# Performance work log

Hardware: AMD Instinct MI355X
Metric: run time of the kernel (lower is better)

The kernel has to match this reference:

```python
import jax, jax.numpy as jnp
import numpy as np

D_MODEL = 512
D_STATE = 128
D_CONV = 4
D_INNER = 1024
HEADDIM = 64
NHEADS = 16
CONV_DIM = D_INNER + 2 * D_STATE          # 1280
D_IN_PROJ = 2 * D_INNER + 2 * D_STATE + NHEADS  # 2320
N_LAYER = 28
VOCAB = 256
EPS = 1e-5
BATCH = 16
SEQ = 768


def _rms(x, w):
    return x * jax.lax.rsqrt(jnp.mean(x * x, axis=-1, keepdims=True) + EPS) * w


def _ssd(x, dt, A, Bm, Cm):
    # x [B,L,H,P], dt [B,L,H], A [H], Bm/Cm [B,L,N] (ngroups=1, broadcast over heads)
    Bb, L, H, P = x.shape
    N = Bm.shape[-1]
    dA = jnp.exp(dt * A)          # [B,L,H] discrete decay
    dBx = dt[..., None] * x       # [B,L,H,P]

    def step(h, t):
        dA_t, dBx_t, B_t, C_t = t
        # h: [B,H,P,N]
        h = dA_t[:, :, None, None] * h + dBx_t[..., None] * B_t[:, None, None, :]
        y = jnp.einsum('bhpn,bn->bhp', h, C_t)
        return h, y

    h0 = jnp.zeros((Bb, H, P, N), x.dtype)
    xs = (jnp.moveaxis(dA, 1, 0), jnp.moveaxis(dBx, 1, 0),
          jnp.moveaxis(Bm, 1, 0), jnp.moveaxis(Cm, 1, 0))
    _, ys = jax.lax.scan(step, h0, xs)
    return jnp.moveaxis(ys, 0, 1)  # [B,L,H,P]


def _mamba2(u, p):
    # u: [B,L,D_MODEL]
    Bb, L, _ = u.shape
    zxbcdt = u @ p['in_proj_w'].T                      # [B,L,2320]
    z = zxbcdt[..., :D_INNER]
    xBC = zxbcdt[..., D_INNER:D_INNER + CONV_DIM]
    dt = jax.nn.softplus(zxbcdt[..., D_INNER + CONV_DIM:] + p['dt_bias'])  # [B,L,H]
    # causal depthwise conv1d (kernel 4) + silu
    xp = jnp.pad(xBC, ((0, 0), (D_CONV - 1, 0), (0, 0)))
    conv = sum(xp[:, k:k + L, :] * p['conv_w'][:, k] for k in range(D_CONV)) + p['conv_b']
    xBC = jax.nn.silu(conv)
    x = xBC[..., :D_INNER].reshape(Bb, L, NHEADS, HEADDIM)
    Bm = xBC[..., D_INNER:D_INNER + D_STATE]
    Cm = xBC[..., D_INNER + D_STATE:]
    A = -jnp.exp(p['A_log'])                           # [H]
    y = _ssd(x, dt, A, Bm, Cm) + p['D'][None, None, :, None] * x
    y = y.reshape(Bb, L, D_INNER)
    # RMSNormGated (norm_before_gate=False): norm(y * silu(z)) * w
    y = _rms(y * jax.nn.silu(z), p['gnorm_w'])
    return y @ p['out_proj_w'].T


def _forward(tokens, targets, params):
    hidden = params['embedding'][tokens]               # [B,L,D]
    residual = jnp.zeros_like(hidden)

    layer_params = {k: params[k] for k in
                    ('in_proj_w', 'conv_w', 'conv_b', 'dt_bias', 'A_log',
                     'D', 'gnorm_w', 'out_proj_w', 'block_norm_w')}

    def layer(carry, lp):
        h, res = carry
        res = h + res
        h = _rms(res, lp['block_norm_w'])
        h = _mamba2(h, lp)
        return (h, res), None

    (hidden, residual), _ = jax.lax.scan(layer, (hidden, residual), layer_params)
    hidden = _rms(hidden + residual, params['norm_f_w'])
    logits = hidden @ params['embedding'].T            # tied lm_head
    logp = jax.nn.log_softmax(logits, axis=-1)
    loss = -jnp.mean(jnp.take_along_axis(logp, targets[..., None], axis=-1))
    return logits, loss


def setup_inputs():
    key = jax.random.key(0)
    ks = jax.random.split(key, 12)
    tokens = jax.random.randint(ks[0], (BATCH, SEQ), 0, VOCAB, dtype=jnp.int32)
    targets = jax.random.randint(ks[1], (BATCH, SEQ), 0, VOCAB, dtype=jnp.int32)
    embedding = jax.random.normal(ks[2], (VOCAB, D_MODEL), jnp.float32) * 0.02
    in_proj_w = jax.random.normal(ks[3], (N_LAYER, D_IN_PROJ, D_MODEL), jnp.float32) * (D_MODEL ** -0.5)
    conv_w = jax.random.normal(ks[4], (N_LAYER, CONV_DIM, D_CONV), jnp.float32) * 0.2
    conv_b = jnp.zeros((N_LAYER, CONV_DIM), jnp.float32)
    dt0 = jnp.exp(jax.random.uniform(ks[5], (N_LAYER, NHEADS)) * (np.log(0.1) - np.log(1e-3)) + np.log(1e-3))
    dt_bias = dt0 + jnp.log(-jnp.expm1(-dt0))          # inverse softplus
    A_log = jnp.log(jax.random.uniform(ks[6], (N_LAYER, NHEADS), minval=1.0, maxval=16.0))
    Dp = jnp.ones((N_LAYER, NHEADS), jnp.float32)
    gnorm_w = jnp.ones((N_LAYER, D_INNER), jnp.float32)
    out_proj_w = jax.random.normal(ks[7], (N_LAYER, D_MODEL, D_INNER), jnp.float32) * (D_INNER ** -0.5 / np.sqrt(N_LAYER))
    block_norm_w = jnp.ones((N_LAYER, D_MODEL), jnp.float32)
    norm_f_w = jnp.ones((D_MODEL,), jnp.float32)
    return {'tokens': tokens, 'targets': targets, 'embedding': embedding,
            'in_proj_w': in_proj_w, 'conv_w': conv_w, 'conv_b': conv_b,
            'dt_bias': dt_bias, 'A_log': A_log, 'D': Dp, 'gnorm_w': gnorm_w,
            'out_proj_w': out_proj_w, 'block_norm_w': block_norm_w, 'norm_f_w': norm_f_w}


def reference(tokens, targets, embedding, in_proj_w, conv_w, conv_b, dt_bias,
              A_log, D, gnorm_w, out_proj_w, block_norm_w, norm_f_w):
    params = {'embedding': embedding, 'in_proj_w': in_proj_w, 'conv_w': conv_w,
              'conv_b': conv_b, 'dt_bias': dt_bias, 'A_log': A_log, 'D': D,
              'gnorm_w': gnorm_w, 'out_proj_w': out_proj_w,
              'block_norm_w': block_norm_w, 'norm_f_w': norm_f_w}
    return _forward(tokens, targets, params)
```

## Files before the change

### kernel.cpp

```cpp
#include <hip/hip_runtime.h>
#include <hip/hip_bf16.h>
#include <math.h>

#define BATCH   16
#define SEQ     768
#define DMODEL  512
#define DSTATE  128
#define DINNER  1024
#define NHEADS  16
#define HEADDIM 64
#define CONVDIM 1280
#define DINPROJ 2320
#define DINPROJP 2432
#define DTBASE  2304
#define NLAYER  28
#define VOCABSZ 256
#define NROWS   (BATCH*SEQ)
#define EPSV    1e-5f
#define NCH     8
#define CH      96
#define STATESZ (HEADDIM*DSTATE)

typedef __hip_bfloat16 bf16_t;
typedef __attribute__((ext_vector_type(8))) __bf16 bf16x8;
typedef __attribute__((ext_vector_type(4))) float floatx4;

__device__ __forceinline__ float siluf(float v) { return v / (1.f + expf(-v)); }

__device__ __forceinline__ void gload_lds16(const bf16_t* g, bf16_t* l) {
  __builtin_amdgcn_global_load_lds(
      (const __attribute__((address_space(1))) unsigned int*)g,
      (__attribute__((address_space(3))) unsigned int*)l, 16, 0, 0);
}

__global__ __launch_bounds__(256) void embed_kernel(const int* __restrict__ tok,
    const float* __restrict__ emb, float* __restrict__ hid, float* __restrict__ res,
    bf16_t* __restrict__ w_emb_bf) {
  int i = blockIdx.x * 256 + threadIdx.x;
  const int total = NROWS * DMODEL;
  if (i < total) {
    int r = i >> 9;
    int d = i & (DMODEL - 1);
    hid[i] = emb[(size_t)tok[r] * DMODEL + d];
    res[i] = 0.f;
  } else {
    int j = i - total;
    if (j < VOCABSZ * DMODEL) w_emb_bf[j] = __float2bfloat16(emb[j]);
  }
}

__global__ __launch_bounds__(256) void cvt_weights_kernel(const float* __restrict__ ipw,
    const float* __restrict__ opw, bf16_t* __restrict__ win, bf16_t* __restrict__ wout) {
  int i = blockIdx.x * 256 + threadIdx.x;
  const int n1 = DINPROJP * DMODEL;
  if (i < n1) {
    int row = i >> 9, col = i & (DMODEL - 1);
    float v = (row < DINPROJ) ? ipw[(size_t)row * DMODEL + col] : 0.f;
    win[i] = __float2bfloat16(v);
  } else {
    int j = i - n1;
    if (j < DMODEL * DINNER) wout[j] = __float2bfloat16(opw[j]);
  }
}

__global__ __launch_bounds__(128) void prenorm_kernel(const float* __restrict__ h,
    float* __restrict__ res, const float* __restrict__ w, bf16_t* __restrict__ xn) {
  int row = blockIdx.x;
  int tid = threadIdx.x;
  const float4* h4 = (const float4*)(h + (size_t)row * DMODEL);
  float4* r4 = (float4*)(res + (size_t)row * DMODEL);
  float4 v = r4[tid];
  float4 a = h4[tid];
  v.x += a.x; v.y += a.y; v.z += a.z; v.w += a.w;
  r4[tid] = v;
  float ss = v.x * v.x + v.y * v.y + v.z * v.z + v.w * v.w;
  #pragma unroll
  for (int o = 32; o > 0; o >>= 1) ss += __shfl_down(ss, o);
  __shared__ float wred[2];
  if ((tid & 63) == 0) wred[tid >> 6] = ss;
  __syncthreads();
  float tot = wred[0] + wred[1];
  float scale = rsqrtf(tot / (float)DMODEL + EPSV);
  const float4* w4 = (const float4*)w;
  float4 wv = w4[tid];
  union { bf16_t b[4]; uint2 u; } pk;
  pk.b[0] = __float2bfloat16(v.x * scale * wv.x);
  pk.b[1] = __float2bfloat16(v.y * scale * wv.y);
  pk.b[2] = __float2bfloat16(v.z * scale * wv.z);
  pk.b[3] = __float2bfloat16(v.w * scale * wv.w);
  ((uint2*)(xn + (size_t)row * DMODEL))[tid] = pk.u;
}

template<int BN, typename TO>
__global__ __launch_bounds__(256) void gemm_bf16_bt(const bf16_t* __restrict__ A,
    const bf16_t* __restrict__ B, TO* __restrict__ C, float* __restrict__ aux,
    int M, int N, int K) {
  constexpr int JF = BN / 32;
  __shared__ bf16_t As[128 * 32];
  __shared__ bf16_t Bs[BN * 32];
  int tid = threadIdx.x;
  int m0 = blockIdx.y * 128;
  int n0 = blockIdx.x * BN;
  int w = tid >> 6, lane = tid & 63;
  int wm = (w >> 1) * 64, wn = (w & 1) * (BN / 2);
  int l16 = lane & 15, lq = lane >> 4;
  floatx4 acc[4][JF];
  #pragma unroll
  for (int i = 0; i < 4; ++i)
    #pragma unroll
    for (int j = 0; j < JF; ++j)
      acc[i][j] = (floatx4){0.f, 0.f, 0.f, 0.f};
  int arow0 = tid >> 2, ak0 = (tid & 3) * 8;
  const bf16_t* Abase = A + (size_t)m0 * K;
  const bf16_t* Bbase = B + (size_t)n0 * K;
  bf16_t* AsW = As + (w << 9);
  bf16_t* BsW = Bs + (w << 9);
  for (int k0 = 0; k0 < K; k0 += 32) {
    __syncthreads();
    gload_lds16(Abase + (size_t)arow0 * K + k0 + ak0, AsW);
    gload_lds16(Abase + (size_t)(arow0 + 64) * K + k0 + ak0, AsW + 2048);
    gload_lds16(Bbase + (size_t)arow0 * K + k0 + ak0, BsW);
    if (BN == 128)
      gload_lds16(Bbase + (size_t)(arow0 + 64) * K + k0 + ak0, BsW + 2048);
    __syncthreads();
    bf16x8 af[4], bfr[JF];
    #pragma unroll
    for (int i = 0; i < 4; ++i)
      af[i] = *(const bf16x8*)(As + (wm + i * 16 + l16) * 32 + lq * 8);
    #pragma unroll
    for (int j = 0; j < JF; ++j)
      bfr[j] = *(const bf16x8*)(Bs + (wn + j * 16 + l16) * 32 + lq * 8);
    #pragma unroll
    for (int i = 0; i < 4; ++i)
      #pragma unroll
      for (int j = 0; j < JF; ++j)
        acc[i][j] = __builtin_amdgcn_mfma_f32_16x16x32_bf16(af[i], bfr[j], acc[i][j], 0, 0, 0);
  }
  #pragma unroll
  for (int i = 0; i < 4; ++i) {
    #pragma unroll
    for (int j = 0; j < JF; ++j) {
      int n = n0 + wn + j * 16 + l16;
      if (n < N) {
        int mb = m0 + wm + i * 16 + lq * 4;
        #pragma unroll
        for (int r = 0; r < 4; ++r) {
          float vv = acc[i][j][r];
          if constexpr (sizeof(TO) == 2)
            C[(size_t)(mb + r) * N + n] = __float2bfloat16(vv);
          else
            C[(size_t)(mb + r) * N + n] = vv;
          if (aux && n >= DTBASE)
            aux[(size_t)(mb + r) * NHEADS + (n - DTBASE)] = vv;
        }
      }
    }
  }
}

__global__ __launch_bounds__(320) void convdt_kernel(const bf16_t* __restrict__ zx,
    const float* __restrict__ dtcol, const float* __restrict__ cw,
    const float* __restrict__ cb, const float* __restrict__ dt_bias,
    const float* __restrict__ A_log, bf16_t* __restrict__ out,
    float* __restrict__ dt, float* __restrict__ ldA) {
  int bl0 = blockIdx.x * 4;
  int t0 = bl0 % SEQ;
  int tid = threadIdx.x;
  int c = tid * 4;
  const bf16_t* base = zx + (size_t)bl0 * DINPROJ + DINNER + c;
  float4 v[7];
  #pragma unroll
  for (int k = 0; k < 7; ++k) {
    int tt = t0 + k - 3;
    if (tt >= 0) {
      union { ushort4 u; bf16_t b[4]; } q;
      q.u = *(const ushort4*)(base + (ptrdiff_t)(k - 3) * DINPROJ);
      v[k] = make_float4(__bfloat162float(q.b[0]), __bfloat162float(q.b[1]),
                         __bfloat162float(q.b[2]), __bfloat162float(q.b[3]));
    } else {
      v[k] = make_float4(0.f, 0.f, 0.f, 0.f);
    }
  }
  float4 w0 = *(const float4*)(cw + (size_t)(c + 0) * 4);
  float4 w1 = *(const float4*)(cw + (size_t)(c + 1) * 4);
  float4 w2 = *(const float4*)(cw + (size_t)(c + 2) * 4);
  float4 w3 = *(const float4*)(cw + (size_t)(c + 3) * 4);
  float4 bias = *(const float4*)(cb + c);
  const float* w0f = (const float*)&w0;
  const float* w1f = (const float*)&w1;
  const float* w2f = (const float*)&w2;
  const float* w3f = (const float*)&w3;
  #pragma unroll
  for (int j = 0; j < 4; ++j) {
    float4 acc = bias;
    #pragma unroll
    for (int k = 0; k < 4; ++k) {
      float4 vv = v[j + k];
      acc.x += vv.x * w0f[k];
      acc.y += vv.y * w1f[k];
      acc.z += vv.z * w2f[k];
      acc.w += vv.w * w3f[k];
    }
    union { ushort4 u; bf16_t b[4]; } pk;
    pk.b[0] = __float2bfloat16(siluf(acc.x));
    pk.b[1] = __float2bfloat16(siluf(acc.y));
    pk.b[2] = __float2bfloat16(siluf(acc.z));
    pk.b[3] = __float2bfloat16(siluf(acc.w));
    *(ushort4*)(out + (size_t)(bl0 + j) * CONVDIM + c) = pk.u;
  }
  if (tid < 64) {
    int j = tid >> 4, h = tid & 15;
    int bl = bl0 + j;
    float vv = dtcol[(size_t)bl * NHEADS + h] + dt_bias[h];
    float sp = fmaxf(vv, 0.f) + log1pf(expf(-fabsf(vv)));
    float Ah = -expf(A_log[h]);
    dt[bl * NHEADS + h] = sp;
    ldA[bl * NHEADS + h] = sp * Ah;
  }
}

__global__ __launch_bounds__(512) void scan_mfma_kernel(const bf16_t* __restrict__ conv,
    const float* __restrict__ dtb, const float* __restrict__ ldAb,
    const float* __restrict__ Dp, float* __restrict__ y,
    float* __restrict__ state, float* __restrict__ chunkprod,
    float* __restrict__ cumb) {
  const int c  = blockIdx.x;
  const int b  = blockIdx.y >> 1;
  const int h0 = (blockIdx.y & 1) * 8;
  const int tid  = threadIdx.x;
  const int w    = tid >> 6;
  const int lane = tid & 63;
  const size_t row0 = (size_t)(b * SEQ + c * CH);

  __shared__ __align__(16) bf16_t Bb[96 * 136];
  __shared__ __align__(16) bf16_t Cb[96 * 136];
  __shared__ __align__(16) bf16_t Pl[96 * 104];
  __shared__ __align__(16) bf16_t xT[64 * 104];
  __shared__ __align__(16) bf16_t BTw[128 * 104];
  __shared__ float ldas[8][96];
  __shared__ float dts[8][96];
  __shared__ float cums[8][96];
  __shared__ float wts[8][96];

  for (int i = tid; i < 96 * 32; i += 512) {
    int t = i >> 5, g = i & 31;
    bf16x8 v = *(const bf16x8*)(conv + (row0 + t) * CONVDIM + DINNER + g * 8);
    if (g < 16) *(bf16x8*)(Bb + t * 136 + g * 8) = v;
    else        *(bf16x8*)(Cb + t * 136 + (g - 16) * 8) = v;
  }
  for (int i = tid; i < 768; i += 512) {
    int hh = i & 7, t = i >> 3;
    size_t gi = (row0 + t) * NHEADS + h0 + hh;
    dts[hh][t]  = dtb[gi];
    ldas[hh][t] = ldAb[gi];
  }
  __syncthreads();
  if (tid < 8) {
    float cacc = 0.f;
    for (int t = 0; t < 96; ++t) { cacc += ldas[tid][t]; cums[tid][t] = cacc; }
  }
  __syncthreads();
  for (int i = tid; i < 768; i += 512) {
    int hh = i & 7, t = i >> 3;
    wts[hh][t] = expf(cums[hh][95] - cums[hh][t]) * dts[hh][t];
    cumb[(row0 + t) * NHEADS + h0 + hh] = cums[hh][t];
  }
  if (tid < 8)
    chunkprod[(b * NHEADS + h0 + tid) * NCH + c] = expf(cums[tid][95]);

  floatx4 gacc[5];
  #pragma unroll
  for (int it = 0; it < 5; ++it) gacc[it] = (floatx4){0.f, 0.f, 0.f, 0.f};
  const int l16 = lane & 15, lk = (lane >> 4) << 3;
  #pragma unroll
  for (int it = 0; it < 5; ++it) {
    int tt = w + it * 8;
    int ti = (tt < 36) ? (tt / 6) : 0;
    int si = (tt < 36) ? (tt % 6) : 0;
    #pragma unroll
    for (int ks = 0; ks < 4; ++ks) {
      bf16x8 a = *(const bf16x8*)(Cb + (ti * 16 + l16) * 136 + ks * 32 + lk);
      bf16x8 bb = *(const bf16x8*)(Bb + (si * 16 + l16) * 136 + ks * 32 + lk);
      gacc[it] = __builtin_amdgcn_mfma_f32_16x16x32_bf16(a, bb, gacc[it], 0, 0, 0);
    }
  }

  for (int hh = 0; hh < 8; ++hh) {
    __syncthreads();
    for (int i = tid; i < 768; i += 512) {
      int t = i >> 3, p8 = (i & 7) * 8;
      union { bf16x8 v8; unsigned short s[8]; } u;
      u.v8 = *(const bf16x8*)(conv + (row0 + t) * CONVDIM + (h0 + hh) * HEADDIM + p8);
      #pragma unroll
      for (int r = 0; r < 8; ++r)
        ((unsigned short*)xT)[(p8 + r) * 104 + t] = u.s[r];
    }
    for (int i = tid; i < 128 * 96; i += 512) {
      int n = i / 96, t = i - n * 96;
      float bv = __bfloat162float(Bb[t * 136 + n]);
      BTw[n * 104 + t] = __float2bfloat16(wts[hh][t] * bv);
    }
    #pragma unroll
    for (int it = 0; it < 5; ++it) {
      int tt = w + it * 8;
      if (tt < 36) {
        int ti = tt / 6, si = tt % 6;
        int scol = si * 16 + l16;
        #pragma unroll
        for (int r = 0; r < 4; ++r) {
          int trow = ti * 16 + ((lane >> 4) << 2) + r;
          float pv = 0.f;
          if (scol <= trow)
            pv = expf(cums[hh][trow] - cums[hh][scol]) * dts[hh][scol] * gacc[it][r];
          Pl[trow * 104 + scol] = __float2bfloat16(pv);
        }
      }
    }
    __syncthreads();
    float Dh = Dp[h0 + hh];
    #pragma unroll
    for (int it = 0; it < 3; ++it) {
      int tt = w + it * 8;
      int ti = tt >> 2, pi = tt & 3;
      floatx4 acc = (floatx4){0.f, 0.f, 0.f, 0.f};
      #pragma unroll
      for (int ks = 0; ks < 3; ++ks) {
        bf16x8 a = *(const bf16x8*)(Pl + (ti * 16 + l16) * 104 + ks * 32 + lk);
        bf16x8 bb = *(const bf16x8*)(xT + (pi * 16 + l16) * 104 + ks * 32 + lk);
        acc = __builtin_amdgcn_mfma_f32_16x16x32_bf16(a, bb, acc, 0, 0, 0);
      }
      int p = pi * 16 + l16;
      #pragma unroll
      for (int r = 0; r < 4; ++r) {
        int t = ti * 16 + ((lane >> 4) << 2) + r;
        float xg = __bfloat162float(conv[(row0 + t) * CONVDIM + (h0 + hh) * HEADDIM + p]);
        y[((row0 + t) * NHEADS + h0 + hh) * HEADDIM + p] = acc[r] + Dh * xg;
      }
    }
    size_t sb = ((size_t)(b * NHEADS + h0 + hh) * NCH + c) * STATESZ;
    #pragma unroll
    for (int it = 0; it < 4; ++it) {
      int tt = w + it * 8;
      int ni = tt >> 2, pi = tt & 3;
      floatx4 acc = (floatx4){0.f, 0.f, 0.f, 0.f};
      #pragma unroll
      for (int ks = 0; ks < 3; ++ks) {
        bf16x8 a = *(const bf16x8*)(BTw + (ni * 16 + l16) * 104 + ks * 32 + lk);
        bf16x8 bb = *(const bf16x8*)(xT + (pi * 16 + l16) * 104 + ks * 32 + lk);
        acc = __builtin_amdgcn_mfma_f32_16x16x32_bf16(a, bb, acc, 0, 0, 0);
      }
      int p = pi * 16 + l16;
      #pragma unroll
      for (int r = 0; r < 4; ++r) {
        int n = ni * 16 + ((lane >> 4) << 2) + r;
        state[sb + (size_t)n * HEADDIM + p] = acc[r];
      }
    }
  }
}

__global__ __launch_bounds__(256) void state_combine_kernel(float* __restrict__ state,
    const float* __restrict__ cprod) {
  int bh = blockIdx.y;
  int sl = blockIdx.x;
  int tid = threadIdx.x;
  float4* slab = (float4*)(state + (size_t)bh * NCH * STATESZ) + sl * 256 + tid;
  const float* pc = cprod + bh * NCH;
  float4 H = make_float4(0.f, 0.f, 0.f, 0.f);
  for (int c = 1; c < NCH; ++c) {
    float P = pc[c - 1];
    float4* sp = slab + (size_t)(c - 1) * (STATESZ / 4);
    float4 S = *sp;
    H.x = P * H.x + S.x; H.y = P * H.y + S.y;
    H.z = P * H.z + S.z; H.w = P * H.w + S.w;
    *sp = H;
  }
}

__global__ __launch_bounds__(512) void ycorr_mfma_kernel(const bf16_t* __restrict__ conv,
    const float* __restrict__ cumb, const float* __restrict__ state,
    float* __restrict__ y) {
  const int c  = blockIdx.x + 1;
  const int b  = blockIdx.y >> 1;
  const int h0 = (blockIdx.y & 1) * 8;
  const int tid  = threadIdx.x;
  const int w    = tid >> 6;
  const int lane = tid & 63;
  const int l16 = lane & 15, lk = (lane >> 4) << 3;
  const size_t row0 = (size_t)(b * SEQ + c * CH);

  __shared__ __align__(16) bf16_t Cb[96 * 136];
  __shared__ __align__(16) bf16_t HT[64 * 136];
  __shared__ float cAs[8][96];

  for (int i = tid; i < 96 * 16; i += 512) {
    int t = i >> 4, g = i & 15;
    bf16x8 v = *(const bf16x8*)(conv + (row0 + t) * CONVDIM + DINNER + DSTATE + g * 8);
    *(bf16x8*)(Cb + t * 136 + g * 8) = v;
  }
  for (int i = tid; i < 768; i += 512) {
    int hh = i & 7, t = i >> 3;
    cAs[hh][t] = expf(cumb[(row0 + t) * NHEADS + h0 + hh]);
  }

  for (int hh = 0; hh < 8; ++hh) {
    __syncthreads();
    const float* Hs = state + ((size_t)(b * NHEADS + h0 + hh) * NCH + (c - 1)) * STATESZ;
    for (int i = tid; i < STATESZ; i += 512) {
      int n = i >> 6, p = i & 63;
      HT[p * 136 + n] = __float2bfloat16(Hs[i]);
    }
    __syncthreads();
    #pragma unroll
    for (int it = 0; it < 3; ++it) {
      int tt = w + it * 8;
      int ti = tt >> 2, pi = tt & 3;
      floatx4 acc = (floatx4){0.f, 0.f, 0.f, 0.f};
      #pragma unroll
      for (int ks = 0; ks < 4; ++ks) {
        bf16x8 a = *(const bf16x8*)(Cb + (ti * 16 + l16) * 136 + ks * 32 + lk);
        bf16x8 bb = *(const bf16x8*)(HT + (pi * 16 + l16) * 136 + ks * 32 + lk);
        acc = __builtin_amdgcn_mfma_f32_16x16x32_bf16(a, bb, acc, 0, 0, 0);
      }
      int p = pi * 16 + l16;
      #pragma unroll
      for (int r = 0; r < 4; ++r) {
        int t = ti * 16 + ((lane >> 4) << 2) + r;
        size_t yi = ((row0 + t) * NHEADS + h0 + hh) * HEADDIM + p;
        y[yi] += cAs[hh][t] * acc[r];
      }
    }
  }
}

__global__ __launch_bounds__(256) void gated_norm_kernel(const float* __restrict__ y,
    const bf16_t* __restrict__ zx, const float* __restrict__ gw, bf16_t* __restrict__ out) {
  int row = blockIdx.x;
  int tid = threadIdx.x;
  const float4* y4 = (const float4*)(y + (size_t)row * DINNER);
  float4 yv = y4[tid];
  union { ushort4 u; bf16_t b[4]; } zq;
  zq.u = ((const ushort4*)(zx + (size_t)row * DINPROJ))[tid];
  float4 zv = make_float4(__bfloat162float(zq.b[0]), __bfloat162float(zq.b[1]),
                          __bfloat162float(zq.b[2]), __bfloat162float(zq.b[3]));
  float4 g;
  g.x = yv.x * siluf(zv.x); g.y = yv.y * siluf(zv.y);
  g.z = yv.z * siluf(zv.z); g.w = yv.w * siluf(zv.w);
  float ss = g.x * g.x + g.y * g.y + g.z * g.z + g.w * g.w;
  #pragma unroll
  for (int o = 32; o > 0; o >>= 1) ss += __shfl_down(ss, o);
  __shared__ float red[4];
  if ((tid & 63) == 0) red[tid >> 6] = ss;
  __syncthreads();
  float tot = red[0] + red[1] + red[2] + red[3];
  float scale = rsqrtf(tot / (float)DINNER + EPSV);
  const float4* g4 = (const float4*)gw;
  float4 wv = g4[tid];
  union { bf16_t b[4]; uint2 u; } pk;
  pk.b[0] = __float2bfloat16(g.x * scale * wv.x);
  pk.b[1] = __float2bfloat16(g.y * scale * wv.y);
  pk.b[2] = __float2bfloat16(g.z * scale * wv.z);
  pk.b[3] = __float2bfloat16(g.w * scale * wv.w);
  ((uint2*)(out + (size_t)row * DINNER))[tid] = pk.u;
}

__global__ __launch_bounds__(256) void rowloss_kernel(const float* __restrict__ logits,
    const int* __restrict__ targets, float* __restrict__ rl) {
  int row = blockIdx.x * 4 + (threadIdx.x >> 6);
  int lane = threadIdx.x & 63;
  const float* lr = logits + (size_t)row * VOCABSZ;
  float4 v = ((const float4*)lr)[lane];
  float mx = fmaxf(fmaxf(v.x, v.y), fmaxf(v.z, v.w));
  #pragma unroll
  for (int o = 32; o > 0; o >>= 1) mx = fmaxf(mx, __shfl_down(mx, o));
  mx = __shfl(mx, 0);
  float e = expf(v.x - mx) + expf(v.y - mx) + expf(v.z - mx) + expf(v.w - mx);
  #pragma unroll
  for (int o = 32; o > 0; o >>= 1) e += __shfl_down(e, o);
  if (lane == 0) {
    float lse = logf(e) + mx;
    rl[row] = lse - lr[targets[row]];
  }
}

__global__ __launch_bounds__(256) void loss_reduce_kernel(const float* __restrict__ rl,
    float* __restrict__ out) {
  int tid = threadIdx.x;
  float ssum = 0.f;
  for (int i = tid; i < NROWS; i += 256) ssum += rl[i];
  #pragma unroll
  for (int o = 32; o > 0; o >>= 1) ssum += __shfl_down(ssum, o);
  __shared__ float red[4];
  if ((tid & 63) == 0) red[tid >> 6] = ssum;
  __syncthreads();
  if (tid == 0) out[0] = (red[0] + red[1] + red[2] + red[3]) / (float)NROWS;
}

extern "C" void kernel_launch(void* const* d_in, const int* in_sizes, int n_in,
                              void* d_out, int out_size, void* d_ws, size_t ws_size,
                              hipStream_t stream) {
  const int*   tokens       = (const int*)d_in[0];
  const int*   targets      = (const int*)d_in[1];
  const float* embedding    = (const float*)d_in[2];
  const float* in_proj_w    = (const float*)d_in[3];
  const float* conv_w       = (const float*)d_in[4];
  const float* conv_b       = (const float*)d_in[5];
  const float* dt_bias      = (const float*)d_in[6];
  const float* A_log        = (const float*)d_in[7];
  const float* Dp           = (const float*)d_in[8];
  const float* gnorm_w      = (const float*)d_in[9];
  const float* out_proj_w   = (const float*)d_in[10];
  const float* block_norm_w = (const float*)d_in[11];
  const float* norm_f_w     = (const float*)d_in[12];
  float* out = (float*)d_out;

  float* ws = (float*)d_ws;
  size_t off = 0;
  float* hidden   = ws + off; off += (size_t)NROWS * DMODEL;
  float* residual = ws + off; off += (size_t)NROWS * DMODEL;
  bf16_t* zx      = (bf16_t*)(ws + off); off += (size_t)NROWS * DINPROJ / 2;
  float* dtcol    = ws + off; off += (size_t)NROWS * NHEADS;
  bf16_t* convo   = (bf16_t*)(ws + off); off += (size_t)NROWS * CONVDIM / 2;
  float* dtb      = ws + off; off += (size_t)NROWS * NHEADS;
  float* ldAb     = ws + off; off += (size_t)NROWS * NHEADS;
  float* cumbuf   = ws + off; off += (size_t)NROWS * NHEADS;
  float* ybuf     = ws + off; off += (size_t)NROWS * DINNER;
  float* cprod    = ws + off; off += (size_t)BATCH * NHEADS * NCH;
  float* rowloss  = ws + off; off += NROWS;
  bf16_t* w_in_bf  = (bf16_t*)(ws + off); off += (size_t)DINPROJP * DMODEL / 2;
  bf16_t* w_out_bf = (bf16_t*)(ws + off); off += (size_t)DMODEL * DINNER / 2;
  bf16_t* w_emb_bf = (bf16_t*)(ws + off); off += (size_t)VOCABSZ * DMODEL / 2;
  float*  state  = ws + off;
  bf16_t* xn_bf  = (bf16_t*)(ws + off);
  bf16_t* yn_bf  = (bf16_t*)(ws + off);
  off += (size_t)BATCH * NHEADS * NCH * STATESZ;

  embed_kernel<<<(NROWS * DMODEL + VOCABSZ * DMODEL) / 256, 256, 0, stream>>>(
      tokens, embedding, hidden, residual, w_emb_bf);

  const int cvt_total = DINPROJP * DMODEL + DMODEL * DINNER;
  for (int l = 0; l < NLAYER; ++l) {
    const float* ipw = in_proj_w + (size_t)l * DINPROJ * DMODEL;
    const float* cw  = conv_w + (size_t)l * CONVDIM * 4;
    const float* cb  = conv_b + (size_t)l * CONVDIM;
    const float* dtbias_l = dt_bias + (size_t)l * NHEADS;
    const float* alog_l   = A_log + (size_t)l * NHEADS;
    const float* D_l      = Dp + (size_t)l * NHEADS;
    const float* gw  = gnorm_w + (size_t)l * DINNER;
    const float* opw = out_proj_w + (size_t)l * DMODEL * DINNER;
    const float* bnw = block_norm_w + (size_t)l * DMODEL;

    cvt_weights_kernel<<<(cvt_total + 255) / 256, 256, 0, stream>>>(ipw, opw, w_in_bf, w_out_bf);
    prenorm_kernel<<<NROWS, 128, 0, stream>>>(hidden, residual, bnw, xn_bf);
    dim3 g1(DINPROJP / 128, NROWS / 128);
    gemm_bf16_bt<128, bf16_t><<<g1, 256, 0, stream>>>(xn_bf, w_in_bf, zx, dtcol,
                                                      NROWS, DINPROJ, DMODEL);
    convdt_kernel<<<NROWS / 4, 320, 0, stream>>>(zx, dtcol, cw, cb, dtbias_l, alog_l,
                                                 convo, dtb, ldAb);
    scan_mfma_kernel<<<dim3(NCH, BATCH * 2), 512, 0, stream>>>(
        convo, dtb, ldAb, D_l, ybuf, state, cprod, cumbuf);
    state_combine_kernel<<<dim3(NCH, BATCH * NHEADS), 256, 0, stream>>>(state, cprod);
    ycorr_mfma_kernel<<<dim3(NCH - 1, BATCH * 2), 512, 0, stream>>>(
        convo, cumbuf, state, ybuf);
    gated_norm_kernel<<<NROWS, 256, 0, stream>>>(ybuf, zx, gw, yn_bf);
    dim3 g2(DMODEL / 64, NROWS / 128);
    gemm_bf16_bt<64, float><<<g2, 256, 0, stream>>>(yn_bf, w_out_bf, hidden, nullptr,
                                                    NROWS, DMODEL, DINNER);
  }

  prenorm_kernel<<<NROWS, 128, 0, stream>>>(hidden, residual, norm_f_w, xn_bf);
  dim3 g3(VOCABSZ / 64, NROWS / 128);
  gemm_bf16_bt<64, float><<<g3, 256, 0, stream>>>(xn_bf, w_emb_bf, out, nullptr,
                                                  NROWS, VOCABSZ, DMODEL);
  rowloss_kernel<<<NROWS / 4, 256, 0, stream>>>(out, targets, rowloss);
  loss_reduce_kernel<<<1, 256, 0, stream>>>(rowloss, out + (size_t)(out_size - 1));
}
```

Baseline: 7.587 ms.

## Hoist weight conversion, emit bf16 combined state, pre-transpose B in scan

Converts all layers' in/out projection weights to bf16 in one launch before the layer loop when workspace allows, removing one conversion kernel per layer. The scan kernel transposes B once per block and applies the decay weights to x instead of rebuilding a weighted B transpose for every head. The state-combine kernel writes the combined states as bf16 into a separate buffer that ycorr reads with vector loads, halving state traffic and dropping the per-element float-to-bf16 conversion there. Costs are extra workspace for all layers' weights, a fallback path if the workspace is too small, and the weighting now rounding x rather than B.

Result: slower. 7.824 ms (+3.1%).

```diff
diff --git a/kernel.cpp b/kernel.cpp
--- a/kernel.cpp
+++ b/kernel.cpp
@@ -63,6 +63,22 @@
   }
 }
 
+__global__ __launch_bounds__(256) void cvt_weights_all_kernel(const float* __restrict__ ipw,
+    const float* __restrict__ opw, bf16_t* __restrict__ win, bf16_t* __restrict__ wout) {
+  size_t i = (size_t)blockIdx.x * 256 + threadIdx.x;
+  const size_t n1 = (size_t)NLAYER * DINPROJP * DMODEL;
+  if (i < n1) {
+    int l = (int)(i / (DINPROJP * DMODEL));
+    int j = (int)(i - (size_t)l * (DINPROJP * DMODEL));
+    int row = j >> 9, col = j & (DMODEL - 1);
+    float v = (row < DINPROJ) ? ipw[(size_t)l * DINPROJ * DMODEL + (size_t)row * DMODEL + col] : 0.f;
+    win[i] = __float2bfloat16(v);
+  } else {
+    size_t j = i - n1;
+    if (j < (size_t)NLAYER * DMODEL * DINNER) wout[j] = __float2bfloat16(opw[j]);
+  }
+}
+
 __global__ __launch_bounds__(128) void prenorm_kernel(const float* __restrict__ h,
     float* __restrict__ res, const float* __restrict__ w, bf16_t* __restrict__ xn) {
   int row = blockIdx.x;
@@ -236,7 +252,8 @@
   __shared__ __align__(16) bf16_t Cb[96 * 136];
   __shared__ __align__(16) bf16_t Pl[96 * 104];
   __shared__ __align__(16) bf16_t xT[64 * 104];
-  __shared__ __align__(16) bf16_t BTw[128 * 104];
+  __shared__ __align__(16) bf16_t xTw[64 * 104];
+  __shared__ __align__(16) bf16_t BT[128 * 104];
   __shared__ float ldas[8][96];
   __shared__ float dts[8][96];
   __shared__ float cums[8][96];
@@ -247,6 +264,14 @@
     bf16x8 v = *(const bf16x8*)(conv + (row0 + t) * CONVDIM + DINNER + g * 8);
     if (g < 16) *(bf16x8*)(Bb + t * 136 + g * 8) = v;
     else        *(bf16x8*)(Cb + t * 136 + (g - 16) * 8) = v;
+  }
+  for (int i = tid; i < 1536; i += 512) {
+    int t = i >> 4, n8 = (i & 15) * 8;
+    union { bf16x8 v8; unsigned short s[8]; } u;
+    u.v8 = *(const bf16x8*)(conv + (row0 + t) * CONVDIM + DINNER + n8);
+    #pragma unroll
+    for (int r = 0; r < 8; ++r)
+      ((unsigned short*)BT)[(n8 + r) * 104 + t] = u.s[r];
   }
   for (int i = tid; i < 768; i += 512) {
     int hh = i & 7, t = i >> 3;
@@ -291,14 +316,12 @@
       int t = i >> 3, p8 = (i & 7) * 8;
       union { bf16x8 v8; unsigned short s[8]; } u;
       u.v8 = *(const bf16x8*)(conv + (row0 + t) * CONVDIM + (h0 + hh) * HEADDIM + p8);
-      #pragma unroll
-      for (int r = 0; r < 8; ++r)
+      float wt = wts[hh][t];
+      #pragma unroll
+      for (int r = 0; r < 8; ++r) {
         ((unsigned short*)xT)[(p8 + r) * 104 + t] = u.s[r];
-    }
-    for (int i = tid; i < 128 * 96; i += 512) {
-      int n = i / 96, t = i - n * 96;
-      float bv = __bfloat162float(Bb[t * 136 + n]);
-      BTw[n * 104 + t] = __float2bfloat16(wts[hh][t] * bv);
+        xTw[(p8 + r) * 104 + t] = __float2bfloat16(wt * (float)u.v8[r]);
+      }
     }
     #pragma unroll
     for (int it = 0; it < 5; ++it) {
@@ -345,8 +368,8 @@
       floatx4 acc = (floatx4){0.f, 0.f, 0.f, 0.f};
       #pragma unroll
       for (int ks = 0; ks < 3; ++ks) {
-        bf16x8 a = *(const bf16x8*)(BTw + (ni * 16 + l16) * 104 + ks * 32 + lk);
-        bf16x8 bb = *(const bf16x8*)(xT + (pi * 16 + l16) * 104 + ks * 32 + lk);
+        bf16x8 a = *(const bf16x8*)(BT + (ni * 16 + l16) * 104 + ks * 32 + lk);
+        bf16x8 bb = *(const bf16x8*)(xTw + (pi * 16 + l16) * 104 + ks * 32 + lk);
         acc = __builtin_amdgcn_mfma_f32_16x16x32_bf16(a, bb, acc, 0, 0, 0);
       }
       int p = pi * 16 + l16;
@@ -359,26 +382,29 @@
   }
 }
 
-__global__ __launch_bounds__(256) void state_combine_kernel(float* __restrict__ state,
-    const float* __restrict__ cprod) {
+__global__ __launch_bounds__(256) void state_combine_kernel(const float* __restrict__ state,
+    const float* __restrict__ cprod, bf16_t* __restrict__ stateT) {
   int bh = blockIdx.y;
   int sl = blockIdx.x;
   int tid = threadIdx.x;
-  float4* slab = (float4*)(state + (size_t)bh * NCH * STATESZ) + sl * 256 + tid;
+  const float4* slab = (const float4*)(state + (size_t)bh * NCH * STATESZ) + sl * 256 + tid;
+  bf16_t* tb = stateT + (size_t)bh * (NCH - 1) * STATESZ + (size_t)(sl * 1024 + tid * 4);
   const float* pc = cprod + bh * NCH;
   float4 H = make_float4(0.f, 0.f, 0.f, 0.f);
   for (int c = 1; c < NCH; ++c) {
     float P = pc[c - 1];
-    float4* sp = slab + (size_t)(c - 1) * (STATESZ / 4);
-    float4 S = *sp;
+    float4 S = slab[(size_t)(c - 1) * (STATESZ / 4)];
     H.x = P * H.x + S.x; H.y = P * H.y + S.y;
     H.z = P * H.z + S.z; H.w = P * H.w + S.w;
-    *sp = H;
+    union { bf16_t b[4]; uint2 u; } pk;
+    pk.b[0] = __float2bfloat16(H.x); pk.b[1] = __float2bfloat16(H.y);
+    pk.b[2] = __float2bfloat16(H.z); pk.b[3] = __float2bfloat16(H.w);
+    *(uint2*)(tb + (size_t)(c - 1) * STATESZ) = pk.u;
   }
 }
 
 __global__ __launch_bounds__(512) void ycorr_mfma_kernel(const bf16_t* __restrict__ conv,
-    const float* __restrict__ cumb, const float* __restrict__ state,
+    const float* __restrict__ cumb, const bf16_t* __restrict__ stateT,
     float* __restrict__ y) {
   const int c  = blockIdx.x + 1;
   const int b  = blockIdx.y >> 1;
@@ -405,10 +431,14 @@
 
   for (int hh = 0; hh < 8; ++hh) {
     __syncthreads();
-    const float* Hs = state + ((size_t)(b * NHEADS + h0 + hh) * NCH + (c - 1)) * STATESZ;
-    for (int i = tid; i < STATESZ; i += 512) {
-      int n = i >> 6, p = i & 63;
-      HT[p * 136 + n] = __float2bfloat16(Hs[i]);
+    const bf16_t* Hs = stateT + ((size_t)(b * NHEADS + h0 + hh) * (NCH - 1) + (c - 1)) * STATESZ;
+    for (int i = tid; i < 1024; i += 512) {
+      int n = i >> 3, p8 = (i & 7) * 8;
+      union { bf16x8 v8; unsigned short s[8]; } u;
+      u.v8 = *(const bf16x8*)(Hs + (size_t)n * HEADDIM + p8);
+      #pragma unroll
+      for (int r = 0; r < 8; ++r)
+        ((unsigned short*)HT)[(p8 + r) * 136 + n] = u.s[r];
     }
     __syncthreads();
     #pragma unroll
@@ -527,16 +557,28 @@
   float* ybuf     = ws + off; off += (size_t)NROWS * DINNER;
   float* cprod    = ws + off; off += (size_t)BATCH * NHEADS * NCH;
   float* rowloss  = ws + off; off += NROWS;
-  bf16_t* w_in_bf  = (bf16_t*)(ws + off); off += (size_t)DINPROJP * DMODEL / 2;
-  bf16_t* w_out_bf = (bf16_t*)(ws + off); off += (size_t)DMODEL * DINNER / 2;
   bf16_t* w_emb_bf = (bf16_t*)(ws + off); off += (size_t)VOCABSZ * DMODEL / 2;
+  bf16_t* stateT  = (bf16_t*)(ws + off); off += (size_t)BATCH * NHEADS * (NCH - 1) * STATESZ / 2;
   float*  state  = ws + off;
   bf16_t* xn_bf  = (bf16_t*)(ws + off);
   bf16_t* yn_bf  = (bf16_t*)(ws + off);
   off += (size_t)BATCH * NHEADS * NCH * STATESZ;
+  bf16_t* w_in_base = (bf16_t*)(ws + off);
+  const size_t in_elems  = (size_t)DINPROJP * DMODEL;
+  const size_t out_elems = (size_t)DMODEL * DINNER;
+  size_t off_all = off + (size_t)NLAYER * (in_elems + out_elems) / 2;
+  bool hoist = ws_size >= off_all * sizeof(float);
+  bf16_t* w_out_all = w_in_base + (size_t)NLAYER * in_elems;
+  bf16_t* w_out_pl  = w_in_base + in_elems;
 
   embed_kernel<<<(NROWS * DMODEL + VOCABSZ * DMODEL) / 256, 256, 0, stream>>>(
       tokens, embedding, hidden, residual, w_emb_bf);
+
+  if (hoist) {
+    size_t total = (size_t)NLAYER * (in_elems + out_elems);
+    cvt_weights_all_kernel<<<(unsigned)((total + 255) / 256), 256, 0, stream>>>(
+        in_proj_w, out_proj_w, w_in_base, w_out_all);
+  }
 
   const int cvt_total = DINPROJP * DMODEL + DMODEL * DINNER;
   for (int l = 0; l < NLAYER; ++l) {
@@ -550,21 +592,25 @@
     const float* opw = out_proj_w + (size_t)l * DMODEL * DINNER;
     const float* bnw = block_norm_w + (size_t)l * DMODEL;
 
-    cvt_weights_kernel<<<(cvt_total + 255) / 256, 256, 0, stream>>>(ipw, opw, w_in_bf, w_out_bf);
+    const bf16_t* wi = hoist ? (w_in_base + (size_t)l * in_elems) : w_in_base;
+    const bf16_t* wo = hoist ? (w_out_all + (size_t)l * out_elems) : w_out_pl;
+    if (!hoist)
+      cvt_weights_kernel<<<(cvt_total + 255) / 256, 256, 0, stream>>>(ipw, opw,
+                                                                      w_in_base, w_out_pl);
     prenorm_kernel<<<NROWS, 128, 0, stream>>>(hidden, residual, bnw, xn_bf);
     dim3 g1(DINPROJP / 128, NROWS / 128);
-    gemm_bf16_bt<128, bf16_t><<<g1, 256, 0, stream>>>(xn_bf, w_in_bf, zx, dtcol,
+    gemm_bf16_bt<128, bf16_t><<<g1, 256, 0, stream>>>(xn_bf, wi, zx, dtcol,
                                                       NROWS, DINPROJ, DMODEL);
     convdt_kernel<<<NROWS / 4, 320, 0, stream>>>(zx, dtcol, cw, cb, dtbias_l, alog_l,
                                                  convo, dtb, ldAb);
     scan_mfma_kernel<<<dim3(NCH, BATCH * 2), 512, 0, stream>>>(
         convo, dtb, ldAb, D_l, ybuf, state, cprod, cumbuf);
-    state_combine_kernel<<<dim3(NCH, BATCH * NHEADS), 256, 0, stream>>>(state, cprod);
+    state_combine_kernel<<<dim3(NCH, BATCH * NHEADS), 256, 0, stream>>>(state, cprod, stateT);
     ycorr_mfma_kernel<<<dim3(NCH - 1, BATCH * 2), 512, 0, stream>>>(
-        convo, cumbuf, state, ybuf);
+        convo, cumbuf, stateT, ybuf);
     gated_norm_kernel<<<NROWS, 256, 0, stream>>>(ybuf, zx, gw, yn_bf);
     dim3 g2(DMODEL / 64, NROWS / 128);
-    gemm_bf16_bt<64, float><<<g2, 256, 0, stream>>>(yn_bf, w_out_bf, hidden, nullptr,
+    gemm_bf16_bt<64, float><<<g2, 256, 0, stream>>>(yn_bf, wo, hidden, nullptr,
                                                     NROWS, DMODEL, DINNER);
   }
 
```
